# Kernel optimization log

Measured on AMD Instinct MI355X. Metric: run time of the kernel, lower is better.

## Reference

```python
import jax, jax.numpy as jnp
import numpy as np

# Sizes matching init_kwargs: r=2, J=3 -> K = 1 + (r-1)*J = 4 framelet operators
N, FEAT, K, NNZ = 20000, 64, 4, 320000
NU, GAMMA, J = 2.0, 1.0, 3  # nu, gamma_0 (gamma never updated on this code path)


def setup_inputs() -> dict:
    key = jax.random.key(0)
    ks = jax.random.split(key, 6)
    F = jax.random.normal(ks[0], (N, FEAT), dtype=jnp.float32)
    w_rows = jax.random.randint(ks[1], (K, NNZ), 0, N, dtype=jnp.int32)
    w_cols = jax.random.randint(ks[2], (K, NNZ), 0, N, dtype=jnp.int32)
    # scale ~1/avg_degree so the 14-step fixed-point iteration is contractive/stable
    w_vals = jax.random.normal(ks[3], (K, NNZ), dtype=jnp.float32) / 16.0
    d = jax.random.uniform(ks[4], (N,), dtype=jnp.float32)
    mask = jax.random.uniform(ks[5], (N, 1), dtype=jnp.float32)
    return {"F": F, "w_rows": w_rows, "w_cols": w_cols, "w_vals": w_vals,
            "d": d, "mask": mask, "thres_iter": 15}


def _spmm(rows, cols, vals, X):
    # sparse [N,N] @ dense [N,FEAT] via gather + segment-sum scatter
    return jax.ops.segment_sum(vals[:, None] * X[cols], rows, num_segments=N)


_spmm_shared = jax.vmap(_spmm, in_axes=(0, 0, 0, None))  # K operators, one dense X
_spmm_each = jax.vmap(_spmm, in_axes=(0, 0, 0, 0))       # K operators, K dense Xs


def _soft(x, thr):  # elementwise soft-thresholding: relu(x-t) - relu(-x-t)
    return jax.nn.relu(x - thr) - jax.nn.relu(-x - thr)


def reference(F, w_rows, w_cols, w_vals, d, mask, thres_iter):
    # nu_jl = [0] + [nu / 4^i for i in range(J)]
    nu = jnp.asarray([0.0] + [NU / (4.0 ** i) for i in range(J)], dtype=jnp.float32)  # [K]
    thr = (nu / GAMMA)[:, None, None] * d[None, :, None]  # [K,N,1] per-operator row thresholds
    d1 = d[:, None]                 # [N,1]
    m2 = mask * mask                # [N,1]
    denom = d1 * m2 + GAMMA         # [N,1]
    num_f = d1 * F * m2             # [N,FEAT]
    Y0 = jnp.zeros((K, N, FEAT), dtype=F.dtype)

    def step(carry, _):
        Uk, Y = carry
        # Z(k+1): soft-threshold of W_jl @ Uk + Y_jl / gamma
        Z = _soft(_spmm_shared(w_rows, w_cols, w_vals, Uk) + Y / GAMMA, thr)  # [K,N,FEAT]
        v = Y - GAMMA * Z
        WTV = _spmm_each(w_rows, w_cols, w_vals, v).sum(axis=0)               # [N,FEAT]
        Uk = (num_f - WTV) / denom
        # Y(k+1) dual update
        Y = Y + GAMMA * (_spmm_shared(w_rows, w_cols, w_vals, Uk) - Z)
        return (Uk, Y), None

    n_iter = int(thres_iter) - 1  # while k < thres_iter starting at k=1
    (Uk, _), _ = jax.lax.scan(jax.checkpoint(step), (F, Y0), None, length=n_iter)
    return Uk
```

## Files before the change

### kernel.cpp

```cpp
#include <hip/hip_runtime.h>


constexpr int N_    = 20000;
constexpr int FEAT_ = 64;
constexpr int K_    = 4;
constexpr int NNZ_  = 320000;
constexpr int NF    = N_ * FEAT_;
constexpr int KN    = K_ * N_;
constexpr int NEDGE = K_ * NNZ_;
constexpr int NITER = 14;
constexpr int BLK   = 256;
constexpr int NSB   = (KN + 255) / 256;
constexpr int NCPY  = 8;
constexpr int NXCD  = 8;
constexpr int EPV   = 2048;
constexpr int NVB   = NEDGE / EPV;

constexpr int R_SP  = 10;
constexpr int NB_SP = ((KN + R_SP - 1) / R_SP + 3) / 4;
constexpr int R_WT  = 4;
constexpr int NB_WT = ((N_ + R_WT - 1) / R_WT + 3) / 4;

__constant__ float c_nu[4] = {0.0f, 2.0f, 0.5f, 0.125f};

__device__ __forceinline__ float softf(float x, float t) {
    float a = fabsf(x) - t;
    a = a > 0.0f ? a : 0.0f;
    return copysignf(a, x);
}

__device__ __forceinline__ float bf2f(unsigned short u) {
    union { unsigned int i; float f; } x;
    x.i = ((unsigned int)u) << 16;
    return x.f;
}
__device__ __forceinline__ unsigned short f2bf(float f) {
    union { float f; unsigned int i; } x;
    x.f = f;
    unsigned int r = x.i + 0x7FFFu + ((x.i >> 16) & 1u);
    return (unsigned short)(r >> 16);
}


__global__ __launch_bounds__(BLK) void precompute_kernel(
    const float* __restrict__ F, const float* __restrict__ d,
    const float* __restrict__ mask, float* __restrict__ dm,
    unsigned short* __restrict__ F_bf) {
    int i = blockIdx.x * BLK + threadIdx.x;
    if (i >= NF / 4) return;
    float4 f = ((const float4*)F)[i];
    ushort4 o;
    o.x = f2bf(f.x); o.y = f2bf(f.y); o.z = f2bf(f.z); o.w = f2bf(f.w);
    ((ushort4*)F_bf)[i] = o;
    if ((i & (FEAT_ / 4 - 1)) == 0) {
        int n = i / (FEAT_ / 4);
        dm[n] = d[n] * mask[n] * mask[n];
    }
}

__global__ __launch_bounds__(BLK) void hist_kernel(
    const int* __restrict__ rows, int* __restrict__ cnt8) {
    int e = blockIdx.x * BLK + threadIdx.x;
    if (e >= NEDGE) return;
    int k = e / NNZ_;
    int copy = blockIdx.x & (NCPY - 1);
    atomicAdd(&cnt8[copy * KN + rows[e] * K_ + k], 1);
}

__global__ __launch_bounds__(256) void scan1_kernel(
    const int* __restrict__ cnt8, int* __restrict__ loc,
    int* __restrict__ bsum) {
    int i = blockIdx.x * 256 + threadIdx.x;
    int x = 0;
    if (i < KN) {
        #pragma unroll
        for (int c = 0; c < NCPY; ++c) x += cnt8[c * KN + i];
    }
    int lane = threadIdx.x & 63, wid = threadIdx.x >> 6;
    int v = x;
    #pragma unroll
    for (int off = 1; off < 64; off <<= 1) {
        int t = __shfl_up(v, off, 64);
        if (lane >= off) v += t;
    }
    __shared__ int ws[4];
    if (lane == 63) ws[wid] = v;
    __syncthreads();
    int add = 0;
    for (int u = 0; u < wid; ++u) add += ws[u];
    v += add;
    if (i < KN) loc[i] = v - x;
    if (threadIdx.x == 255) bsum[blockIdx.x] = v;
}

__global__ __launch_bounds__(512) void scan2_kernel(int* __restrict__ bsum) {
    int tid = threadIdx.x;
    int x = (tid < NSB) ? bsum[tid] : 0;
    int lane = tid & 63, wid = tid >> 6;
    int v = x;
    #pragma unroll
    for (int off = 1; off < 64; off <<= 1) {
        int t = __shfl_up(v, off, 64);
        if (lane >= off) v += t;
    }
    __shared__ int ws[8];
    if (lane == 63) ws[wid] = v;
    __syncthreads();
    int add = 0;
    for (int u = 0; u < wid; ++u) add += ws[u];
    v += add;
    if (tid < NSB) bsum[tid] = v - x;
}

__global__ __launch_bounds__(256) void scan3_kernel(
    const int* __restrict__ loc, const int* __restrict__ bsum,
    int* __restrict__ offs, int* __restrict__ cursor) {
    int i = blockIdx.x * 256 + threadIdx.x;
    if (i < KN) {
        int v = loc[i] + bsum[blockIdx.x];
        offs[i] = v;
        cursor[i] = v;
    }
    if (i == 0) offs[KN] = NEDGE;
}

__global__ __launch_bounds__(BLK) void scatter_kernel(
    const int* __restrict__ rows, const int* __restrict__ cols,
    const float* __restrict__ vals, int* __restrict__ cursor,
    unsigned int* __restrict__ cmeta) {
    int xcd = blockIdx.x & (NXCD - 1);
    int vb  = blockIdx.x >> 3;
    int ebase = vb * EPV;
    #pragma unroll
    for (int i = 0; i < EPV / BLK; ++i) {
        int e = ebase + i * BLK + threadIdx.x;
        int row = rows[e];
        if (row / (N_ / NXCD) != xcd) continue;
        int k = e / NNZ_;
        unsigned int b  = __float_as_uint(vals[e]);
        unsigned int rb = b + 0x1FFFu + ((b >> 14) & 1u);
        int exp8 = (int)((rb >> 23) & 0xFF);
        unsigned int pk = 0u;
        if (exp8 > 96)
            pk = (b & 0x80000000u) | ((unsigned int)(exp8 - 96) << 26) |
                 (((rb >> 14) & 0x1FFu) << 17);
        pk |= ((unsigned int)k << 15) | (unsigned int)cols[e];
        int pos = atomicAdd(&cursor[row * K_ + k], 1);
        cmeta[pos] = pk;
    }
}


template <int BATCH>
__device__ __forceinline__ void row_accum_bf(
    const unsigned int* __restrict__ cmeta, const ushort4* __restrict__ Xb,
    int beg, int end, int lane, int sub, int q, int padc, float4& acc) {
    for (int ebase = beg; ebase < end; ebase += 64) {
        int n = end - ebase;
        if (n > 64) n = 64;
        int   c_l = padc;
        float v_l = 0.0f;
        if (lane < n) {
            unsigned int p = cmeta[ebase + lane];
            c_l = (int)((p >> 15) & 3u) * N_ + (int)(p & 0x7FFFu);
            unsigned int e5 = (p >> 26) & 0x1Fu;
            unsigned int bits = (p & 0x80000000u) | ((e5 + 96u) << 23) |
                                (((p >> 17) & 0x1FFu) << 14);
            v_l = (e5 == 0u) ? 0.0f : __uint_as_float(bits);
        }
        int iters = (n + 3) >> 2;
        int itersPad = (iters + BATCH - 1) & ~(BATCH - 1);
        for (int it0 = 0; it0 < itersPad; it0 += BATCH) {
            float   vv[BATCH];
            ushort4 xx[BATCH];
            #pragma unroll
            for (int u = 0; u < BATCH; ++u) {
                int j = 4 * (it0 + u) + sub;
                int   c = __shfl(c_l, j, 64);
                vv[u]   = __shfl(v_l, j, 64);
                xx[u]   = Xb[c * (FEAT_ / 4) + q];
            }
            #pragma unroll
            for (int u = 0; u < BATCH; ++u) {
                acc.x += vv[u] * bf2f(xx[u].x);
                acc.y += vv[u] * bf2f(xx[u].y);
                acc.z += vv[u] * bf2f(xx[u].z);
                acc.w += vv[u] * bf2f(xx[u].w);
            }
        }
    }
}

__device__ __forceinline__ void butterfly4(float4& a) {
    #pragma unroll
    for (int m = 16; m <= 32; m <<= 1) {
        a.x += __shfl_xor(a.x, m, 64);
        a.y += __shfl_xor(a.y, m, 64);
        a.z += __shfl_xor(a.z, m, 64);
        a.w += __shfl_xor(a.w, m, 64);
    }
}

template <bool FIRST>
__global__ __launch_bounds__(BLK) void spmm_fused_kernel(
    const int* __restrict__ offs, const unsigned int* __restrict__ cmeta,
    const unsigned short* __restrict__ Xb,
    const float* __restrict__ d, unsigned short* __restrict__ V_bf) {
    int wave = (blockIdx.x * BLK + threadIdx.x) >> 6;
    int lane = threadIdx.x & 63;
    int sub  = lane >> 4, q = lane & 15;
    int base = wave * R_SP;
    if (base >= KN) return;
    int off_l = 0;
    if (lane <= R_SP) {
        int i = base + lane;
        if (i > KN) i = KN;
        off_l = offs[i];
    }
    const ushort4* X4 = (const ushort4*)Xb;
    ushort4* V4 = (ushort4*)V_bf;
    for (int r = 0; r < R_SP; ++r) {
        int w = base + r;
        if (w >= KN) break;
        int k = w & (K_ - 1);
        int n = w >> 2;
        int beg = __shfl(off_l, r, 64);
        int end = __shfl(off_l, r + 1, 64);
        const ushort4* X4m = X4 - (size_t)k * N_ * (FEAT_ / 4);
        float4 acc = {0.f, 0.f, 0.f, 0.f};
        row_accum_bf<4>(cmeta, X4m, beg, end, lane, sub, q, k * N_, acc);
        butterfly4(acc);
        if (sub == 0) {
            int idx4 = (k * N_ + n) * (FEAT_ / 4) + q;
            float thr = c_nu[k] * d[n];
            float4 y;
            if (FIRST) {
                y = make_float4(0.f, 0.f, 0.f, 0.f);
            } else {
                ushort4 vp = V4[idx4];
                y.x = acc.x + bf2f(vp.x); y.y = acc.y + bf2f(vp.y);
                y.z = acc.z + bf2f(vp.z); y.w = acc.w + bf2f(vp.w);
            }
            ushort4 o;
            o.x = f2bf(y.x - softf(acc.x + y.x, thr));
            o.y = f2bf(y.y - softf(acc.y + y.y, thr));
            o.z = f2bf(y.z - softf(acc.z + y.z, thr));
            o.w = f2bf(y.w - softf(acc.w + y.w, thr));
            V4[idx4] = o;
        }
    }
}

__global__ __launch_bounds__(BLK) void wtv_u_kernel(
    const int* __restrict__ offs, const unsigned int* __restrict__ cmeta,
    const unsigned short* __restrict__ V_bf,
    const float* __restrict__ F, const float* __restrict__ dm,
    float* __restrict__ U, unsigned short* __restrict__ U_bf) {
    int wave = (blockIdx.x * BLK + threadIdx.x) >> 6;
    int lane = threadIdx.x & 63;
    int sub  = lane >> 4, q = lane & 15;
    int base = wave * R_WT;
    if (base >= N_) return;
    int off_l = 0;
    if (lane <= K_ * R_WT) {
        int i = K_ * base + lane;
        if (i > KN) i = KN;
        off_l = offs[i];
    }
    const ushort4* V4 = (const ushort4*)V_bf;
    for (int r = 0; r < R_WT; ++r) {
        int n = base + r;
        if (n >= N_) break;
        int beg = __shfl(off_l, K_ * r, 64);
        int end = __shfl(off_l, K_ * r + K_, 64);
        float4 acc = {0.f, 0.f, 0.f, 0.f};
        row_accum_bf<8>(cmeta, V4, beg, end, lane, sub, q, 0, acc);
        butterfly4(acc);
        if (sub == 0) {
            int idx4 = n * (FEAT_ / 4) + q;
            float dmv = dm[n];
            float r2 = 1.0f / (dmv + 1.0f);
            float4 f = ((const float4*)F)[idx4];
            float4 o;
            o.x = (dmv * f.x - acc.x) * r2; o.y = (dmv * f.y - acc.y) * r2;
            o.z = (dmv * f.z - acc.z) * r2; o.w = (dmv * f.w - acc.w) * r2;
            ((float4*)U)[idx4] = o;
            ushort4 ob;
            ob.x = f2bf(o.x); ob.y = f2bf(o.y);
            ob.z = f2bf(o.z); ob.w = f2bf(o.w);
            ((ushort4*)U_bf)[idx4] = ob;
        }
    }
}

extern "C" void kernel_launch(void* const* d_in, const int* in_sizes, int n_in,
                              void* d_out, int out_size, void* d_ws, size_t ws_size,
                              hipStream_t stream) {
    const float* F      = (const float*)d_in[0];
    const int*   w_rows = (const int*)d_in[1];
    const int*   w_cols = (const int*)d_in[2];
    const float* w_vals = (const float*)d_in[3];
    const float* d      = (const float*)d_in[4];
    const float* mask   = (const float*)d_in[5];
    float* U = (float*)d_out;

    unsigned int* cmeta  = (unsigned int*)d_ws;
    unsigned short* V_bf = (unsigned short*)(cmeta + NEDGE);
    unsigned short* U_bf = V_bf + (size_t)KN * FEAT_;
    unsigned short* F_bf = U_bf + NF;
    float* dm     = (float*)(F_bf + NF);
    int*   cnt8   = (int*)(dm + N_);
    int*   loc    = cnt8 + NCPY * KN;
    int*   bsum   = loc + KN;
    int*   offs   = bsum + 512;
    int*   cursor = offs + KN + 1;

    const int gEdge = NEDGE / BLK;
    const int gNF4  = (NF / 4) / BLK;

    hipMemsetAsync(cnt8, 0, (size_t)NCPY * KN * 4, stream);
    precompute_kernel<<<gNF4, BLK, 0, stream>>>(F, d, mask, dm, F_bf);
    hist_kernel<<<gEdge, BLK, 0, stream>>>(w_rows, cnt8);
    scan1_kernel<<<NSB, 256, 0, stream>>>(cnt8, loc, bsum);
    scan2_kernel<<<1, 512, 0, stream>>>(bsum);
    scan3_kernel<<<NSB, 256, 0, stream>>>(loc, bsum, offs, cursor);
    scatter_kernel<<<NVB * NXCD, BLK, 0, stream>>>(w_rows, w_cols, w_vals,
                                                   cursor, cmeta);

    spmm_fused_kernel<true><<<NB_SP, BLK, 0, stream>>>(offs, cmeta, F_bf, d, V_bf);
    for (int it = 0; it < NITER; ++it) {
        wtv_u_kernel<<<NB_WT, BLK, 0, stream>>>(offs, cmeta, V_bf,
                                                F, dm, U, U_bf);
        if (it < NITER - 1)
            spmm_fused_kernel<false><<<NB_SP, BLK, 0, stream>>>(offs, cmeta,
                                                                U_bf, d, V_bf);
    }
}
```

Before: 929.9 us.

## Switch SpMM gathers to lane-per-feature with uniform edge metadata and bf16 values

Edge metadata is repacked so the upper 15 bits hold a truncated bf16-like weight and the lower 17 bits a combined k*N+col index, which removes the custom exponent encoding and its decode. The SpMM and WtV kernels now assign one feature per lane over the full 64-wide row and walk edges serially with wave-uniform loads. This removes the shuffles and the cross-subgroup butterfly reduction. In exchange each gathered row is read as 64 scalar bf16 loads instead of 16 ushort4 loads spread over 4 edges, and the edge weights carry slightly less mantissa precision.

```diff
diff --git a/kernel.cpp b/kernel.cpp
--- a/kernel.cpp
+++ b/kernel.cpp
@@ -138,13 +138,9 @@
         if (row / (N_ / NXCD) != xcd) continue;
         int k = e / NNZ_;
         unsigned int b  = __float_as_uint(vals[e]);
-        unsigned int rb = b + 0x1FFFu + ((b >> 14) & 1u);
-        int exp8 = (int)((rb >> 23) & 0xFF);
-        unsigned int pk = 0u;
-        if (exp8 > 96)
-            pk = (b & 0x80000000u) | ((unsigned int)(exp8 - 96) << 26) |
-                 (((rb >> 14) & 0x1FFu) << 17);
-        pk |= ((unsigned int)k << 15) | (unsigned int)cols[e];
+        unsigned int rb = b + 0xFFFFu + ((b >> 17) & 1u);
+        unsigned int pk = (rb & 0xFFFE0000u) |
+                          (unsigned int)(k * N_ + cols[e]);
         int pos = atomicAdd(&cursor[row * K_ + k], 1);
         cmeta[pos] = pk;
     }
@@ -152,52 +148,20 @@
 
 
 template <int BATCH>
-__device__ __forceinline__ void row_accum_bf(
-    const unsigned int* __restrict__ cmeta, const ushort4* __restrict__ Xb,
-    int beg, int end, int lane, int sub, int q, int padc, float4& acc) {
-    for (int ebase = beg; ebase < end; ebase += 64) {
-        int n = end - ebase;
-        if (n > 64) n = 64;
-        int   c_l = padc;
-        float v_l = 0.0f;
-        if (lane < n) {
-            unsigned int p = cmeta[ebase + lane];
-            c_l = (int)((p >> 15) & 3u) * N_ + (int)(p & 0x7FFFu);
-            unsigned int e5 = (p >> 26) & 0x1Fu;
-            unsigned int bits = (p & 0x80000000u) | ((e5 + 96u) << 23) |
-                                (((p >> 17) & 0x1FFu) << 14);
-            v_l = (e5 == 0u) ? 0.0f : __uint_as_float(bits);
+__device__ __forceinline__ void seg_accum(
+    const unsigned int* __restrict__ cmeta,
+    const unsigned short* __restrict__ Xb,
+    int beg, int end, int lane, float& acc) {
+    for (int e = beg; e < end; e += BATCH) {
+        #pragma unroll
+        for (int j = 0; j < BATCH; ++j) {
+            int a = e + j;
+            bool valid = a < end;
+            unsigned int p = cmeta[valid ? a : beg];
+            float v = valid ? __uint_as_float(p & 0xFFFE0000u) : 0.0f;
+            int   c = (int)(p & 0x1FFFFu);
+            acc += v * bf2f(Xb[(size_t)c * FEAT_ + lane]);
         }
-        int iters = (n + 3) >> 2;
-        int itersPad = (iters + BATCH - 1) & ~(BATCH - 1);
-        for (int it0 = 0; it0 < itersPad; it0 += BATCH) {
-            float   vv[BATCH];
-            ushort4 xx[BATCH];
-            #pragma unroll
-            for (int u = 0; u < BATCH; ++u) {
-                int j = 4 * (it0 + u) + sub;
-                int   c = __shfl(c_l, j, 64);
-                vv[u]   = __shfl(v_l, j, 64);
-                xx[u]   = Xb[c * (FEAT_ / 4) + q];
-            }
-            #pragma unroll
-            for (int u = 0; u < BATCH; ++u) {
-                acc.x += vv[u] * bf2f(xx[u].x);
-                acc.y += vv[u] * bf2f(xx[u].y);
-                acc.z += vv[u] * bf2f(xx[u].z);
-                acc.w += vv[u] * bf2f(xx[u].w);
-            }
-        }
-    }
-}
-
-__device__ __forceinline__ void butterfly4(float4& a) {
-    #pragma unroll
-    for (int m = 16; m <= 32; m <<= 1) {
-        a.x += __shfl_xor(a.x, m, 64);
-        a.y += __shfl_xor(a.y, m, 64);
-        a.z += __shfl_xor(a.z, m, 64);
-        a.w += __shfl_xor(a.w, m, 64);
     }
 }
 
@@ -206,48 +170,26 @@
     const int* __restrict__ offs, const unsigned int* __restrict__ cmeta,
     const unsigned short* __restrict__ Xb,
     const float* __restrict__ d, unsigned short* __restrict__ V_bf) {
-    int wave = (blockIdx.x * BLK + threadIdx.x) >> 6;
     int lane = threadIdx.x & 63;
-    int sub  = lane >> 4, q = lane & 15;
+    int wave = __builtin_amdgcn_readfirstlane(
+        (int)((blockIdx.x * BLK + threadIdx.x) >> 6));
     int base = wave * R_SP;
     if (base >= KN) return;
-    int off_l = 0;
-    if (lane <= R_SP) {
-        int i = base + lane;
-        if (i > KN) i = KN;
-        off_l = offs[i];
-    }
-    const ushort4* X4 = (const ushort4*)Xb;
-    ushort4* V4 = (ushort4*)V_bf;
     for (int r = 0; r < R_SP; ++r) {
         int w = base + r;
         if (w >= KN) break;
         int k = w & (K_ - 1);
         int n = w >> 2;
-        int beg = __shfl(off_l, r, 64);
-        int end = __shfl(off_l, r + 1, 64);
-        const ushort4* X4m = X4 - (size_t)k * N_ * (FEAT_ / 4);
-        float4 acc = {0.f, 0.f, 0.f, 0.f};
-        row_accum_bf<4>(cmeta, X4m, beg, end, lane, sub, q, k * N_, acc);
-        butterfly4(acc);
-        if (sub == 0) {
-            int idx4 = (k * N_ + n) * (FEAT_ / 4) + q;
-            float thr = c_nu[k] * d[n];
-            float4 y;
-            if (FIRST) {
-                y = make_float4(0.f, 0.f, 0.f, 0.f);
-            } else {
-                ushort4 vp = V4[idx4];
-                y.x = acc.x + bf2f(vp.x); y.y = acc.y + bf2f(vp.y);
-                y.z = acc.z + bf2f(vp.z); y.w = acc.w + bf2f(vp.w);
-            }
-            ushort4 o;
-            o.x = f2bf(y.x - softf(acc.x + y.x, thr));
-            o.y = f2bf(y.y - softf(acc.y + y.y, thr));
-            o.z = f2bf(y.z - softf(acc.z + y.z, thr));
-            o.w = f2bf(y.w - softf(acc.w + y.w, thr));
-            V4[idx4] = o;
-        }
+        int beg = offs[w];
+        int end = offs[w + 1];
+        const unsigned short* Xm = Xb - (size_t)k * N_ * FEAT_;
+        float acc = 0.0f;
+        seg_accum<4>(cmeta, Xm, beg, end, lane, acc);
+        int idx = (k * N_ + n) * FEAT_ + lane;
+        float thr = c_nu[k] * d[n];
+        float y = FIRST ? 0.0f : (acc + bf2f(V_bf[idx]));
+        float z = softf(acc + y, thr);
+        V_bf[idx] = f2bf(y - z);
     }
 }
 
@@ -256,40 +198,24 @@
     const unsigned short* __restrict__ V_bf,
     const float* __restrict__ F, const float* __restrict__ dm,
     float* __restrict__ U, unsigned short* __restrict__ U_bf) {
-    int wave = (blockIdx.x * BLK + threadIdx.x) >> 6;
     int lane = threadIdx.x & 63;
-    int sub  = lane >> 4, q = lane & 15;
+    int wave = __builtin_amdgcn_readfirstlane(
+        (int)((blockIdx.x * BLK + threadIdx.x) >> 6));
     int base = wave * R_WT;
     if (base >= N_) return;
-    int off_l = 0;
-    if (lane <= K_ * R_WT) {
-        int i = K_ * base + lane;
-        if (i > KN) i = KN;
-        off_l = offs[i];
-    }
-    const ushort4* V4 = (const ushort4*)V_bf;
     for (int r = 0; r < R_WT; ++r) {
         int n = base + r;
         if (n >= N_) break;
-        int beg = __shfl(off_l, K_ * r, 64);
-        int end = __shfl(off_l, K_ * r + K_, 64);
-        float4 acc = {0.f, 0.f, 0.f, 0.f};
-        row_accum_bf<8>(cmeta, V4, beg, end, lane, sub, q, 0, acc);
-        butterfly4(acc);
-        if (sub == 0) {
-            int idx4 = n * (FEAT_ / 4) + q;
-            float dmv = dm[n];
-            float r2 = 1.0f / (dmv + 1.0f);
-            float4 f = ((const float4*)F)[idx4];
-            float4 o;
-            o.x = (dmv * f.x - acc.x) * r2; o.y = (dmv * f.y - acc.y) * r2;
-            o.z = (dmv * f.z - acc.z) * r2; o.w = (dmv * f.w - acc.w) * r2;
-            ((float4*)U)[idx4] = o;
-            ushort4 ob;
-            ob.x = f2bf(o.x); ob.y = f2bf(o.y);
-            ob.z = f2bf(o.z); ob.w = f2bf(o.w);
-            ((ushort4*)U_bf)[idx4] = ob;
-        }
+        int beg = offs[K_ * n];
+        int end = offs[K_ * n + K_];
+        float acc = 0.0f;
+        seg_accum<8>(cmeta, V_bf, beg, end, lane, acc);
+        int idx = n * FEAT_ + lane;
+        float dmv = dm[n];
+        float r2 = 1.0f / (dmv + 1.0f);
+        float o = (dmv * F[idx] - acc) * r2;
+        U[idx] = o;
+        U_bf[idx] = f2bf(o);
     }
 }
 
```

After: 1.503 ms. +61.6%, slower.
